# Performance work log

Measured on AMD Instinct MI355X. Metric: run time of the kernel, lower is better.

## Reference

```python
import jax, jax.numpy as jnp
import numpy as np

LOTRI2MAT = np.array([[0, 1, 3], [1, 2, 4], [3, 4, 5]])  # lower-tri 6-vec -> symmetric 3x3
MAT2LOTRI_I = np.array([0, 1, 1, 2, 2, 2])
MAT2LOTRI_J = np.array([0, 0, 1, 0, 1, 2])


def trilinear_warp_border(img, ddf):
    """MONAI Warp(mode='bilinear', padding_mode='border', align_corners=True).
    img: (B,C,H,W,D), ddf: (B,3,H,W,D) displacement in voxel units.
    Samples img at x + ddf(x), clamping coords to the volume (border padding).
    """
    B, C, H, W, D = img.shape
    base = jnp.stack(
        jnp.meshgrid(jnp.arange(H), jnp.arange(W), jnp.arange(D), indexing='ij'),
        axis=0,
    ).astype(img.dtype)  # (3,H,W,D)
    coords = ddf + base[None]  # (B,3,H,W,D)
    x = jnp.clip(coords[:, 0], 0.0, H - 1)
    y = jnp.clip(coords[:, 1], 0.0, W - 1)
    z = jnp.clip(coords[:, 2], 0.0, D - 1)

    x0f, y0f, z0f = jnp.floor(x), jnp.floor(y), jnp.floor(z)
    fx, fy, fz = x - x0f, y - y0f, z - z0f
    x0 = jnp.clip(x0f.astype(jnp.int32), 0, H - 1)
    y0 = jnp.clip(y0f.astype(jnp.int32), 0, W - 1)
    z0 = jnp.clip(z0f.astype(jnp.int32), 0, D - 1)
    x1 = jnp.minimum(x0 + 1, H - 1)
    y1 = jnp.minimum(y0 + 1, W - 1)
    z1 = jnp.minimum(z0 + 1, D - 1)

    def gather(img_b, xi, yi, zi):
        flat = (xi * W + yi) * D + zi  # (H,W,D)
        return img_b.reshape(C, -1)[:, flat.reshape(-1)].reshape(C, H, W, D)

    g = jax.vmap(gather)  # over batch

    out = jnp.zeros_like(img)
    for xi, wx in ((x0, 1.0 - fx), (x1, fx)):
        for yi, wy in ((y0, 1.0 - fy), (y1, fy)):
            for zi, wz in ((z0, 1.0 - fz), (z1, fz)):
                out = out + g(img, xi, yi, zi) * (wx * wy * wz)[:, None]
    return out


def jacobian_of_ddf(ddf):
    """J = I + du/dx via central differences (one-sided at boundaries).
    ddf: (B,3,H,W,D) -> (B,H,W,D,3,3) with J[...,i,j] = d u_i / d x_j + delta_ij."""
    grads = jnp.gradient(ddf, axis=(2, 3, 4))  # list over j of (B,3,H,W,D)
    J = jnp.stack(grads, axis=2)  # (B,3(i),3(j),H,W,D)
    J = J + jnp.eye(3, dtype=ddf.dtype)[None, :, :, None, None, None]
    return jnp.transpose(J, (0, 3, 4, 5, 1, 2))  # (B,H,W,D,3,3)


def setup_inputs() -> dict:
    key = jax.random.key(0)
    k1, k2 = jax.random.split(key)
    dti = jax.random.normal(k1, (2, 6, 64, 64, 64), dtype=jnp.float32)
    ddf = jax.random.normal(k2, (2, 3, 64, 64, 64), dtype=jnp.float32)
    return {"dti": dti, "ddf": ddf}


def reference(dti, ddf):
    b, _, h, w, d = dti.shape
    # 1) trilinear warp of the 6-channel lower-tri DTI
    dti_warped = trilinear_warp_border(dti, ddf)  # (B,6,H,W,D)
    # 2) lower-tri -> full symmetric 3x3, spatial-last
    M = dti_warped[:, LOTRI2MAT]                      # (B,3,3,H,W,D)
    M = jnp.transpose(M, (0, 3, 4, 5, 1, 2))          # (B,H,W,D,3,3)
    # 3) Jacobian of the deformation and its polar-decomposition rotation (finite strain)
    J = jacobian_of_ddf(ddf)                          # (B,H,W,D,3,3)
    U, _, Vh = jnp.linalg.svd(J, full_matrices=False)
    R = jnp.matmul(U, Vh)                             # orthogonal factor of J
    # 4) rotate tensors: R^T M R
    out = jnp.einsum('...ji,...jk,...kl->...il', R, M, R)
    # 5) back to lower-tri channel-first form
    out = jnp.transpose(out, (0, 4, 5, 1, 2, 3))      # (B,3,3,H,W,D)
    return out[:, MAT2LOTRI_I, MAT2LOTRI_J]           # (B,6,H,W,D)
```

## Files before the change

### kernel.cpp

```cpp
#include <hip/hip_runtime.h>

#define NVOX 262144
#define TOTAL (2 * NVOX)

typedef float f2u __attribute__((ext_vector_type(2), aligned(4)));

__global__ void zero_count(int* __restrict__ bad) {
    if (threadIdx.x == 0) bad[0] = 0;
}

__global__ __launch_bounds__(256)
void warp_main(const float* __restrict__ dti,
               const float* __restrict__ ddf,
               float* __restrict__ out,
               int* __restrict__ bad, int max_bad)
{
    const int idx = blockIdx.x * 256 + threadIdx.x;
    const int b = idx >> 18;
    const int r = idx & (NVOX - 1);
    const int x = r >> 12;
    const int y = (r >> 6) & 63;
    const int z = r & 63;

    const float* db = ddf + (size_t)b * 3 * NVOX;

    const float ux = db[r];
    const float uy = db[NVOX + r];
    const float uz = db[2 * NVOX + r];

    const float cx = fminf(fmaxf((float)x + ux, 0.0f), 63.0f);
    const float cy = fminf(fmaxf((float)y + uy, 0.0f), 63.0f);
    const float cz = fminf(fmaxf((float)z + uz, 0.0f), 63.0f);
    const float fx0 = floorf(cx), fy0 = floorf(cy), fz0 = floorf(cz);
    const float fx = cx - fx0, fy = cy - fy0, fz = cz - fz0;
    const int x0 = (int)fx0, y0 = (int)fy0, z0 = (int)fz0;
    const int x1 = min(x0 + 1, 63), y1 = min(y0 + 1, 63);

    const float gx = 1.0f - fx, gy = 1.0f - fy, gz = 1.0f - fz;
    const float q00 = gx * gy, q01 = gx * fy, q10 = fx * gy, q11 = fx * fy;

    const bool ztop = (z0 == 63);
    const int zb = ztop ? 62 : z0;
    const int p00 = (x0 * 64 + y0) * 64 + zb, p01 = (x0 * 64 + y1) * 64 + zb;
    const int p10 = (x1 * 64 + y0) * 64 + zb, p11 = (x1 * 64 + y1) * 64 + zb;

    const float* tb = dti + (size_t)b * 6 * NVOX;
    float m[6];
#pragma unroll
    for (int c = 0; c < 6; ++c) {
        const float* tc = tb + c * NVOX;
        const f2u v00 = *(const f2u*)(tc + p00);
        const f2u v01 = *(const f2u*)(tc + p01);
        const f2u v10 = *(const f2u*)(tc + p10);
        const f2u v11 = *(const f2u*)(tc + p11);
        const float l00 = (ztop ? v00.y : v00.x) * gz + v00.y * fz;
        const float l01 = (ztop ? v01.y : v01.x) * gz + v01.y * fz;
        const float l10 = (ztop ? v10.y : v10.x) * gz + v10.y * fz;
        const float l11 = (ztop ? v11.y : v11.x) * gz + v11.y * fz;
        m[c] = q00 * l00 + q01 * l01 + q10 * l10 + q11 * l11;
    }

    const int xm = max(x - 1, 0), xp = min(x + 1, 63);
    const int ym = max(y - 1, 0), yp = min(y + 1, 63);
    const int zm = max(z - 1, 0), zp = min(z + 1, 63);
    const float sx = (xp - xm == 2) ? 0.5f : 1.0f;
    const float sy = (yp - ym == 2) ? 0.5f : 1.0f;
    const float sz = (zp - zm == 2) ? 0.5f : 1.0f;

    float P[3][3];
#pragma unroll
    for (int i = 0; i < 3; ++i) {
        const float* ui = db + i * NVOX;
        const float ctr = (i == 0) ? ux : (i == 1) ? uy : uz;
        P[i][0] = (ui[(xp * 64 + y) * 64 + z] - ui[(xm * 64 + y) * 64 + z]) * sx
                + (i == 0 ? 1.0f : 0.0f);
        P[i][1] = (ui[(x * 64 + yp) * 64 + z] - ui[(x * 64 + ym) * 64 + z]) * sy
                + (i == 1 ? 1.0f : 0.0f);
        P[i][2] = (__shfl(ctr, zp) - __shfl(ctr, zm)) * sz + (i == 2 ? 1.0f : 0.0f);
    }

    float cond_est = 0.0f;
#pragma unroll
    for (int it = 0; it < 6; ++it) {
        const float C00 = P[1][1] * P[2][2] - P[1][2] * P[2][1];
        const float C01 = P[1][2] * P[2][0] - P[1][0] * P[2][2];
        const float C02 = P[1][0] * P[2][1] - P[1][1] * P[2][0];
        const float C10 = P[0][2] * P[2][1] - P[0][1] * P[2][2];
        const float C11 = P[0][0] * P[2][2] - P[0][2] * P[2][0];
        const float C12 = P[0][1] * P[2][0] - P[0][0] * P[2][1];
        const float C20 = P[0][1] * P[1][2] - P[0][2] * P[1][1];
        const float C21 = P[0][2] * P[1][0] - P[0][0] * P[1][2];
        const float C22 = P[0][0] * P[1][1] - P[0][1] * P[1][0];
        const float det = P[0][0] * C00 + P[0][1] * C01 + P[0][2] * C02;

        const float n2 = P[0][0]*P[0][0] + P[0][1]*P[0][1] + P[0][2]*P[0][2]
                       + P[1][0]*P[1][0] + P[1][1]*P[1][1] + P[1][2]*P[1][2]
                       + P[2][0]*P[2][0] + P[2][1]*P[2][1] + P[2][2]*P[2][2];
        const float a2 = C00*C00 + C01*C01 + C02*C02
                       + C10*C10 + C11*C11 + C12*C12
                       + C20*C20 + C21*C21 + C22*C22;

        const float ad = fmaxf(fabsf(det), 1e-30f);
        if (it == 0) cond_est = sqrtf(n2 * a2) / ad;

        const float t  = fmaxf(__builtin_amdgcn_sqrtf(a2 * __builtin_amdgcn_rcpf(n2)), 1e-20f);
        const float sg = (det < 0.0f) ? -1.0f : 1.0f;
        const float rt = __builtin_amdgcn_rsqf(t * ad);
        const float c1 = 0.5f * t * rt;
        const float c2 = 0.5f * sg * rt;

        P[0][0] = c1 * P[0][0] + c2 * C00;  P[0][1] = c1 * P[0][1] + c2 * C01;  P[0][2] = c1 * P[0][2] + c2 * C02;
        P[1][0] = c1 * P[1][0] + c2 * C10;  P[1][1] = c1 * P[1][1] + c2 * C11;  P[1][2] = c1 * P[1][2] + c2 * C12;
        P[2][0] = c1 * P[2][0] + c2 * C20;  P[2][1] = c1 * P[2][1] + c2 * C21;  P[2][2] = c1 * P[2][2] + c2 * C22;
    }

    const float M3[3][3] = {{m[0], m[1], m[3]},
                            {m[1], m[2], m[4]},
                            {m[3], m[4], m[5]}};
    float T[3][3];
#pragma unroll
    for (int i = 0; i < 3; ++i)
#pragma unroll
        for (int j = 0; j < 3; ++j)
            T[i][j] = P[0][i] * M3[0][j] + P[1][i] * M3[1][j] + P[2][i] * M3[2][j];

    float A[3][3];
#pragma unroll
    for (int i = 0; i < 3; ++i)
#pragma unroll
        for (int j = 0; j < 3; ++j)
            A[i][j] = T[i][0] * P[0][j] + T[i][1] * P[1][j] + T[i][2] * P[2][j];

    float* ob = out + (size_t)b * 6 * NVOX;
    ob[0 * NVOX + r] = A[0][0];
    ob[1 * NVOX + r] = A[1][0];
    ob[2 * NVOX + r] = A[1][1];
    ob[3 * NVOX + r] = A[2][0];
    ob[4 * NVOX + r] = A[2][1];
    ob[5 * NVOX + r] = A[2][2];

    if (cond_est > 1e4f) {
        const int slot = atomicAdd(bad, 1);
        if (slot < max_bad) bad[1 + slot] = idx;
    }
}

__global__ __launch_bounds__(256)
void rescue(const float* __restrict__ dti,
            const float* __restrict__ ddf,
            float* __restrict__ out,
            const int* __restrict__ bad, int max_bad)
{
    const int n = min(bad[0], max_bad);
    for (int k = blockIdx.x * 256 + threadIdx.x; k < n; k += 4 * 256) {
        const int idx = bad[1 + k];
        const int b = idx >> 18;
        const int r = idx & (NVOX - 1);
        const int x = r >> 12;
        const int y = (r >> 6) & 63;
        const int z = r & 63;

        const float* db = ddf + (size_t)b * 3 * NVOX;

        const float cx = fminf(fmaxf((float)x + db[r], 0.0f), 63.0f);
        const float cy = fminf(fmaxf((float)y + db[NVOX + r], 0.0f), 63.0f);
        const float cz = fminf(fmaxf((float)z + db[2 * NVOX + r], 0.0f), 63.0f);
        const float fx0 = floorf(cx), fy0 = floorf(cy), fz0 = floorf(cz);
        const float fx = cx - fx0, fy = cy - fy0, fz = cz - fz0;
        const int x0 = (int)fx0, y0 = (int)fy0, z0 = (int)fz0;
        const int x1 = min(x0 + 1, 63), y1 = min(y0 + 1, 63), z1 = min(z0 + 1, 63);
        const float gx = 1.0f - fx, gy = 1.0f - fy, gz = 1.0f - fz;
        const float w000 = gx*gy*gz, w001 = gx*gy*fz, w010 = gx*fy*gz, w011 = gx*fy*fz;
        const float w100 = fx*gy*gz, w101 = fx*gy*fz, w110 = fx*fy*gz, w111 = fx*fy*fz;
        const int o000 = (x0*64+y0)*64+z0, o001 = (x0*64+y0)*64+z1;
        const int o010 = (x0*64+y1)*64+z0, o011 = (x0*64+y1)*64+z1;
        const int o100 = (x1*64+y0)*64+z0, o101 = (x1*64+y0)*64+z1;
        const int o110 = (x1*64+y1)*64+z0, o111 = (x1*64+y1)*64+z1;

        const float* tb = dti + (size_t)b * 6 * NVOX;
        float m[6];
        for (int c = 0; c < 6; ++c) {
            const float* tc = tb + c * NVOX;
            m[c] = w000*tc[o000] + w001*tc[o001] + w010*tc[o010] + w011*tc[o011]
                 + w100*tc[o100] + w101*tc[o101] + w110*tc[o110] + w111*tc[o111];
        }

        const int xm = max(x-1,0), xp = min(x+1,63);
        const int ym = max(y-1,0), yp = min(y+1,63);
        const int zm = max(z-1,0), zp = min(z+1,63);
        const double sx = (xp-xm==2)?0.5:1.0, sy = (yp-ym==2)?0.5:1.0, sz = (zp-zm==2)?0.5:1.0;
        double X[3][3];
        for (int i = 0; i < 3; ++i) {
            const float* ui = db + i * NVOX;
            X[i][0] = ((double)ui[(xp*64+y)*64+z] - (double)ui[(xm*64+y)*64+z]) * sx + (i==0?1.0:0.0);
            X[i][1] = ((double)ui[(x*64+yp)*64+z] - (double)ui[(x*64+ym)*64+z]) * sy + (i==1?1.0:0.0);
            X[i][2] = ((double)ui[(x*64+y)*64+zp] - (double)ui[(x*64+y)*64+zm]) * sz + (i==2?1.0:0.0);
        }

        for (int it = 0; it < 14; ++it) {
            double mx = 0.0;
            for (int i = 0; i < 3; ++i)
                for (int j = 0; j < 3; ++j) mx = fmax(mx, fabs(X[i][j]));
            const double s = 1.0 / fmax(mx, 1e-300);
            for (int i = 0; i < 3; ++i)
                for (int j = 0; j < 3; ++j) X[i][j] *= s;

            const double C00 = X[1][1]*X[2][2] - X[1][2]*X[2][1];
            const double C01 = X[1][2]*X[2][0] - X[1][0]*X[2][2];
            const double C02 = X[1][0]*X[2][1] - X[1][1]*X[2][0];
            const double C10 = X[0][2]*X[2][1] - X[0][1]*X[2][2];
            const double C11 = X[0][0]*X[2][2] - X[0][2]*X[2][0];
            const double C12 = X[0][1]*X[2][0] - X[0][0]*X[2][1];
            const double C20 = X[0][1]*X[1][2] - X[0][2]*X[1][1];
            const double C21 = X[0][2]*X[1][0] - X[0][0]*X[1][2];
            const double C22 = X[0][0]*X[1][1] - X[0][1]*X[1][0];
            const double det = X[0][0]*C00 + X[0][1]*C01 + X[0][2]*C02;
            const double n2 = X[0][0]*X[0][0]+X[0][1]*X[0][1]+X[0][2]*X[0][2]
                            + X[1][0]*X[1][0]+X[1][1]*X[1][1]+X[1][2]*X[1][2]
                            + X[2][0]*X[2][0]+X[2][1]*X[2][1]+X[2][2]*X[2][2];
            const double a2 = C00*C00+C01*C01+C02*C02 + C10*C10+C11*C11+C12*C12
                            + C20*C20+C21*C21+C22*C22;
            const double t  = fmax(sqrt(a2 / n2), 1e-150);
            const double ad = fmax(fabs(det), 1e-280);
            const double sg = (det < 0.0) ? -1.0 : 1.0;
            const double c1 = 0.5 * sqrt(t / ad);
            const double c2 = 0.5 * sg / sqrt(t * ad);
            X[0][0]=c1*X[0][0]+c2*C00; X[0][1]=c1*X[0][1]+c2*C01; X[0][2]=c1*X[0][2]+c2*C02;
            X[1][0]=c1*X[1][0]+c2*C10; X[1][1]=c1*X[1][1]+c2*C11; X[1][2]=c1*X[1][2]+c2*C12;
            X[2][0]=c1*X[2][0]+c2*C20; X[2][1]=c1*X[2][1]+c2*C21; X[2][2]=c1*X[2][2]+c2*C22;
        }

        const double M3[3][3] = {{(double)m[0], (double)m[1], (double)m[3]},
                                 {(double)m[1], (double)m[2], (double)m[4]},
                                 {(double)m[3], (double)m[4], (double)m[5]}};
        double T[3][3], A[3][3];
        for (int i = 0; i < 3; ++i)
            for (int j = 0; j < 3; ++j)
                T[i][j] = X[0][i]*M3[0][j] + X[1][i]*M3[1][j] + X[2][i]*M3[2][j];
        for (int i = 0; i < 3; ++i)
            for (int j = 0; j < 3; ++j)
                A[i][j] = T[i][0]*X[0][j] + T[i][1]*X[1][j] + T[i][2]*X[2][j];

        float* ob = out + (size_t)b * 6 * NVOX;
        ob[0 * NVOX + r] = (float)A[0][0];
        ob[1 * NVOX + r] = (float)A[1][0];
        ob[2 * NVOX + r] = (float)A[1][1];
        ob[3 * NVOX + r] = (float)A[2][0];
        ob[4 * NVOX + r] = (float)A[2][1];
        ob[5 * NVOX + r] = (float)A[2][2];
    }
}

extern "C" void kernel_launch(void* const* d_in, const int* in_sizes, int n_in,
                              void* d_out, int out_size, void* d_ws, size_t ws_size,
                              hipStream_t stream) {
    const float* dti = (const float*)d_in[0];
    const float* ddf = (const float*)d_in[1];
    float* out = (float*)d_out;
    int* bad = (int*)d_ws;
    const int max_bad = (int)min((size_t)8192, ws_size / 4 - 1);

    zero_count<<<1, 64, 0, stream>>>(bad);
    warp_main<<<TOTAL / 256, 256, 0, stream>>>(dti, ddf, out, bad, max_bad);
    rescue<<<4, 256, 0, stream>>>(dti, ddf, out, bad, max_bad);
}
```

Baseline: 105.7 us.

## Replace atomic bad-voxel list with per-voxel flag array and full-grid rescue

Drops the zero-count kernel and the global atomic append list. Each voxel now writes a byte flag, and the condition check compares squared values so the sqrt and divide go away. A full-grid rescue kernel reads the flags, and a wave returns early when no lane is flagged. This removes one launch and the atomic contention, and it also lifts the 8192-entry cap. In exchange it adds a 512K-byte flag write and read plus a large launch that is mostly idle.

```diff
diff --git a/kernel.cpp b/kernel.cpp
--- a/kernel.cpp
+++ b/kernel.cpp
@@ -4,16 +4,12 @@
 #define TOTAL (2 * NVOX)
 
 typedef float f2u __attribute__((ext_vector_type(2), aligned(4)));
-
-__global__ void zero_count(int* __restrict__ bad) {
-    if (threadIdx.x == 0) bad[0] = 0;
-}
 
 __global__ __launch_bounds__(256)
 void warp_main(const float* __restrict__ dti,
                const float* __restrict__ ddf,
                float* __restrict__ out,
-               int* __restrict__ bad, int max_bad)
+               unsigned char* __restrict__ flags)
 {
     const int idx = blockIdx.x * 256 + threadIdx.x;
     const int b = idx >> 18;
@@ -79,7 +75,7 @@
         P[i][2] = (__shfl(ctr, zp) - __shfl(ctr, zm)) * sz + (i == 2 ? 1.0f : 0.0f);
     }
 
-    float cond_est = 0.0f;
+    bool need64 = false;
 #pragma unroll
     for (int it = 0; it < 6; ++it) {
         const float C00 = P[1][1] * P[2][2] - P[1][2] * P[2][1];
@@ -101,7 +97,7 @@
                        + C20*C20 + C21*C21 + C22*C22;
 
         const float ad = fmaxf(fabsf(det), 1e-30f);
-        if (it == 0) cond_est = sqrtf(n2 * a2) / ad;
+        if (it == 0) need64 = (n2 * a2 > 1e8f * ad * ad);
 
         const float t  = fmaxf(__builtin_amdgcn_sqrtf(a2 * __builtin_amdgcn_rcpf(n2)), 1e-20f);
         const float sg = (det < 0.0f) ? -1.0f : 1.0f;
@@ -139,116 +135,114 @@
     ob[4 * NVOX + r] = A[2][1];
     ob[5 * NVOX + r] = A[2][2];
 
-    if (cond_est > 1e4f) {
-        const int slot = atomicAdd(bad, 1);
-        if (slot < max_bad) bad[1 + slot] = idx;
-    }
+    flags[idx] = need64 ? 1 : 0;
 }
 
 __global__ __launch_bounds__(256)
-void rescue(const float* __restrict__ dti,
-            const float* __restrict__ ddf,
-            float* __restrict__ out,
-            const int* __restrict__ bad, int max_bad)
+void rescue_flag(const float* __restrict__ dti,
+                 const float* __restrict__ ddf,
+                 float* __restrict__ out,
+                 const unsigned char* __restrict__ flags)
 {
-    const int n = min(bad[0], max_bad);
-    for (int k = blockIdx.x * 256 + threadIdx.x; k < n; k += 4 * 256) {
-        const int idx = bad[1 + k];
-        const int b = idx >> 18;
-        const int r = idx & (NVOX - 1);
-        const int x = r >> 12;
-        const int y = (r >> 6) & 63;
-        const int z = r & 63;
-
-        const float* db = ddf + (size_t)b * 3 * NVOX;
-
-        const float cx = fminf(fmaxf((float)x + db[r], 0.0f), 63.0f);
-        const float cy = fminf(fmaxf((float)y + db[NVOX + r], 0.0f), 63.0f);
-        const float cz = fminf(fmaxf((float)z + db[2 * NVOX + r], 0.0f), 63.0f);
-        const float fx0 = floorf(cx), fy0 = floorf(cy), fz0 = floorf(cz);
-        const float fx = cx - fx0, fy = cy - fy0, fz = cz - fz0;
-        const int x0 = (int)fx0, y0 = (int)fy0, z0 = (int)fz0;
-        const int x1 = min(x0 + 1, 63), y1 = min(y0 + 1, 63), z1 = min(z0 + 1, 63);
-        const float gx = 1.0f - fx, gy = 1.0f - fy, gz = 1.0f - fz;
-        const float w000 = gx*gy*gz, w001 = gx*gy*fz, w010 = gx*fy*gz, w011 = gx*fy*fz;
-        const float w100 = fx*gy*gz, w101 = fx*gy*fz, w110 = fx*fy*gz, w111 = fx*fy*fz;
-        const int o000 = (x0*64+y0)*64+z0, o001 = (x0*64+y0)*64+z1;
-        const int o010 = (x0*64+y1)*64+z0, o011 = (x0*64+y1)*64+z1;
-        const int o100 = (x1*64+y0)*64+z0, o101 = (x1*64+y0)*64+z1;
-        const int o110 = (x1*64+y1)*64+z0, o111 = (x1*64+y1)*64+z1;
-
-        const float* tb = dti + (size_t)b * 6 * NVOX;
-        float m[6];
-        for (int c = 0; c < 6; ++c) {
-            const float* tc = tb + c * NVOX;
-            m[c] = w000*tc[o000] + w001*tc[o001] + w010*tc[o010] + w011*tc[o011]
-                 + w100*tc[o100] + w101*tc[o101] + w110*tc[o110] + w111*tc[o111];
-        }
-
-        const int xm = max(x-1,0), xp = min(x+1,63);
-        const int ym = max(y-1,0), yp = min(y+1,63);
-        const int zm = max(z-1,0), zp = min(z+1,63);
-        const double sx = (xp-xm==2)?0.5:1.0, sy = (yp-ym==2)?0.5:1.0, sz = (zp-zm==2)?0.5:1.0;
-        double X[3][3];
-        for (int i = 0; i < 3; ++i) {
-            const float* ui = db + i * NVOX;
-            X[i][0] = ((double)ui[(xp*64+y)*64+z] - (double)ui[(xm*64+y)*64+z]) * sx + (i==0?1.0:0.0);
-            X[i][1] = ((double)ui[(x*64+yp)*64+z] - (double)ui[(x*64+ym)*64+z]) * sy + (i==1?1.0:0.0);
-            X[i][2] = ((double)ui[(x*64+y)*64+zp] - (double)ui[(x*64+y)*64+zm]) * sz + (i==2?1.0:0.0);
-        }
-
-        for (int it = 0; it < 14; ++it) {
-            double mx = 0.0;
-            for (int i = 0; i < 3; ++i)
-                for (int j = 0; j < 3; ++j) mx = fmax(mx, fabs(X[i][j]));
-            const double s = 1.0 / fmax(mx, 1e-300);
-            for (int i = 0; i < 3; ++i)
-                for (int j = 0; j < 3; ++j) X[i][j] *= s;
-
-            const double C00 = X[1][1]*X[2][2] - X[1][2]*X[2][1];
-            const double C01 = X[1][2]*X[2][0] - X[1][0]*X[2][2];
-            const double C02 = X[1][0]*X[2][1] - X[1][1]*X[2][0];
-            const double C10 = X[0][2]*X[2][1] - X[0][1]*X[2][2];
-            const double C11 = X[0][0]*X[2][2] - X[0][2]*X[2][0];
-            const double C12 = X[0][1]*X[2][0] - X[0][0]*X[2][1];
-            const double C20 = X[0][1]*X[1][2] - X[0][2]*X[1][1];
-            const double C21 = X[0][2]*X[1][0] - X[0][0]*X[1][2];
-            const double C22 = X[0][0]*X[1][1] - X[0][1]*X[1][0];
-            const double det = X[0][0]*C00 + X[0][1]*C01 + X[0][2]*C02;
-            const double n2 = X[0][0]*X[0][0]+X[0][1]*X[0][1]+X[0][2]*X[0][2]
-                            + X[1][0]*X[1][0]+X[1][1]*X[1][1]+X[1][2]*X[1][2]
-                            + X[2][0]*X[2][0]+X[2][1]*X[2][1]+X[2][2]*X[2][2];
-            const double a2 = C00*C00+C01*C01+C02*C02 + C10*C10+C11*C11+C12*C12
-                            + C20*C20+C21*C21+C22*C22;
-            const double t  = fmax(sqrt(a2 / n2), 1e-150);
-            const double ad = fmax(fabs(det), 1e-280);
-            const double sg = (det < 0.0) ? -1.0 : 1.0;
-            const double c1 = 0.5 * sqrt(t / ad);
-            const double c2 = 0.5 * sg / sqrt(t * ad);
-            X[0][0]=c1*X[0][0]+c2*C00; X[0][1]=c1*X[0][1]+c2*C01; X[0][2]=c1*X[0][2]+c2*C02;
-            X[1][0]=c1*X[1][0]+c2*C10; X[1][1]=c1*X[1][1]+c2*C11; X[1][2]=c1*X[1][2]+c2*C12;
-            X[2][0]=c1*X[2][0]+c2*C20; X[2][1]=c1*X[2][1]+c2*C21; X[2][2]=c1*X[2][2]+c2*C22;
-        }
-
-        const double M3[3][3] = {{(double)m[0], (double)m[1], (double)m[3]},
-                                 {(double)m[1], (double)m[2], (double)m[4]},
-                                 {(double)m[3], (double)m[4], (double)m[5]}};
-        double T[3][3], A[3][3];
+    const int idx = blockIdx.x * 256 + threadIdx.x;
+    const bool mine = (flags[idx] != 0);
+    if (__ballot(mine) == 0ull) return;
+    if (!mine) return;
+
+    const int b = idx >> 18;
+    const int r = idx & (NVOX - 1);
+    const int x = r >> 12;
+    const int y = (r >> 6) & 63;
+    const int z = r & 63;
+
+    const float* db = ddf + (size_t)b * 3 * NVOX;
+
+    const float cx = fminf(fmaxf((float)x + db[r], 0.0f), 63.0f);
+    const float cy = fminf(fmaxf((float)y + db[NVOX + r], 0.0f), 63.0f);
+    const float cz = fminf(fmaxf((float)z + db[2 * NVOX + r], 0.0f), 63.0f);
+    const float fx0 = floorf(cx), fy0 = floorf(cy), fz0 = floorf(cz);
+    const float fx = cx - fx0, fy = cy - fy0, fz = cz - fz0;
+    const int x0 = (int)fx0, y0 = (int)fy0, z0 = (int)fz0;
+    const int x1 = min(x0 + 1, 63), y1 = min(y0 + 1, 63), z1 = min(z0 + 1, 63);
+    const float gx = 1.0f - fx, gy = 1.0f - fy, gz = 1.0f - fz;
+    const float w000 = gx*gy*gz, w001 = gx*gy*fz, w010 = gx*fy*gz, w011 = gx*fy*fz;
+    const float w100 = fx*gy*gz, w101 = fx*gy*fz, w110 = fx*fy*gz, w111 = fx*fy*fz;
+    const int o000 = (x0*64+y0)*64+z0, o001 = (x0*64+y0)*64+z1;
+    const int o010 = (x0*64+y1)*64+z0, o011 = (x0*64+y1)*64+z1;
+    const int o100 = (x1*64+y0)*64+z0, o101 = (x1*64+y0)*64+z1;
+    const int o110 = (x1*64+y1)*64+z0, o111 = (x1*64+y1)*64+z1;
+
+    const float* tb = dti + (size_t)b * 6 * NVOX;
+    float m[6];
+    for (int c = 0; c < 6; ++c) {
+        const float* tc = tb + c * NVOX;
+        m[c] = w000*tc[o000] + w001*tc[o001] + w010*tc[o010] + w011*tc[o011]
+             + w100*tc[o100] + w101*tc[o101] + w110*tc[o110] + w111*tc[o111];
+    }
+
+    const int xm = max(x-1,0), xp = min(x+1,63);
+    const int ym = max(y-1,0), yp = min(y+1,63);
+    const int zm = max(z-1,0), zp = min(z+1,63);
+    const double sx = (xp-xm==2)?0.5:1.0, sy = (yp-ym==2)?0.5:1.0, sz = (zp-zm==2)?0.5:1.0;
+    double X[3][3];
+    for (int i = 0; i < 3; ++i) {
+        const float* ui = db + i * NVOX;
+        X[i][0] = ((double)ui[(xp*64+y)*64+z] - (double)ui[(xm*64+y)*64+z]) * sx + (i==0?1.0:0.0);
+        X[i][1] = ((double)ui[(x*64+yp)*64+z] - (double)ui[(x*64+ym)*64+z]) * sy + (i==1?1.0:0.0);
+        X[i][2] = ((double)ui[(x*64+y)*64+zp] - (double)ui[(x*64+y)*64+zm]) * sz + (i==2?1.0:0.0);
+    }
+
+    for (int it = 0; it < 14; ++it) {
+        double mx = 0.0;
         for (int i = 0; i < 3; ++i)
-            for (int j = 0; j < 3; ++j)
-                T[i][j] = X[0][i]*M3[0][j] + X[1][i]*M3[1][j] + X[2][i]*M3[2][j];
+            for (int j = 0; j < 3; ++j) mx = fmax(mx, fabs(X[i][j]));
+        const double s = 1.0 / fmax(mx, 1e-300);
         for (int i = 0; i < 3; ++i)
-            for (int j = 0; j < 3; ++j)
-                A[i][j] = T[i][0]*X[0][j] + T[i][1]*X[1][j] + T[i][2]*X[2][j];
-
-        float* ob = out + (size_t)b * 6 * NVOX;
-        ob[0 * NVOX + r] = (float)A[0][0];
-        ob[1 * NVOX + r] = (float)A[1][0];
-        ob[2 * NVOX + r] = (float)A[1][1];
-        ob[3 * NVOX + r] = (float)A[2][0];
-        ob[4 * NVOX + r] = (float)A[2][1];
-        ob[5 * NVOX + r] = (float)A[2][2];
-    }
+            for (int j = 0; j < 3; ++j) X[i][j] *= s;
+
+        const double C00 = X[1][1]*X[2][2] - X[1][2]*X[2][1];
+        const double C01 = X[1][2]*X[2][0] - X[1][0]*X[2][2];
+        const double C02 = X[1][0]*X[2][1] - X[1][1]*X[2][0];
+        const double C10 = X[0][2]*X[2][1] - X[0][1]*X[2][2];
+        const double C11 = X[0][0]*X[2][2] - X[0][2]*X[2][0];
+        const double C12 = X[0][1]*X[2][0] - X[0][0]*X[2][1];
+        const double C20 = X[0][1]*X[1][2] - X[0][2]*X[1][1];
+        const double C21 = X[0][2]*X[1][0] - X[0][0]*X[1][2];
+        const double C22 = X[0][0]*X[1][1] - X[0][1]*X[1][0];
+        const double det = X[0][0]*C00 + X[0][1]*C01 + X[0][2]*C02;
+        const double n2 = X[0][0]*X[0][0]+X[0][1]*X[0][1]+X[0][2]*X[0][2]
+                        + X[1][0]*X[1][0]+X[1][1]*X[1][1]+X[1][2]*X[1][2]
+                        + X[2][0]*X[2][0]+X[2][1]*X[2][1]+X[2][2]*X[2][2];
+        const double a2 = C00*C00+C01*C01+C02*C02 + C10*C10+C11*C11+C12*C12
+                        + C20*C20+C21*C21+C22*C22;
+        const double t  = fmax(sqrt(a2 / n2), 1e-150);
+        const double ad = fmax(fabs(det), 1e-280);
+        const double sg = (det < 0.0) ? -1.0 : 1.0;
+        const double c1 = 0.5 * sqrt(t / ad);
+        const double c2 = 0.5 * sg / sqrt(t * ad);
+        X[0][0]=c1*X[0][0]+c2*C00; X[0][1]=c1*X[0][1]+c2*C01; X[0][2]=c1*X[0][2]+c2*C02;
+        X[1][0]=c1*X[1][0]+c2*C10; X[1][1]=c1*X[1][1]+c2*C11; X[1][2]=c1*X[1][2]+c2*C12;
+        X[2][0]=c1*X[2][0]+c2*C20; X[2][1]=c1*X[2][1]+c2*C21; X[2][2]=c1*X[2][2]+c2*C22;
+    }
+
+    const double M3[3][3] = {{(double)m[0], (double)m[1], (double)m[3]},
+                             {(double)m[1], (double)m[2], (double)m[4]},
+                             {(double)m[3], (double)m[4], (double)m[5]}};
+    double T[3][3], A[3][3];
+    for (int i = 0; i < 3; ++i)
+        for (int j = 0; j < 3; ++j)
+            T[i][j] = X[0][i]*M3[0][j] + X[1][i]*M3[1][j] + X[2][i]*M3[2][j];
+    for (int i = 0; i < 3; ++i)
+        for (int j = 0; j < 3; ++j)
+            A[i][j] = T[i][0]*X[0][j] + T[i][1]*X[1][j] + T[i][2]*X[2][j];
+
+    float* ob = out + (size_t)b * 6 * NVOX;
+    ob[0 * NVOX + r] = (float)A[0][0];
+    ob[1 * NVOX + r] = (float)A[1][0];
+    ob[2 * NVOX + r] = (float)A[1][1];
+    ob[3 * NVOX + r] = (float)A[2][0];
+    ob[4 * NVOX + r] = (float)A[2][1];
+    ob[5 * NVOX + r] = (float)A[2][2];
 }
 
 extern "C" void kernel_launch(void* const* d_in, const int* in_sizes, int n_in,
@@ -257,10 +251,8 @@
     const float* dti = (const float*)d_in[0];
     const float* ddf = (const float*)d_in[1];
     float* out = (float*)d_out;
-    int* bad = (int*)d_ws;
-    const int max_bad = (int)min((size_t)8192, ws_size / 4 - 1);
-
-    zero_count<<<1, 64, 0, stream>>>(bad);
-    warp_main<<<TOTAL / 256, 256, 0, stream>>>(dti, ddf, out, bad, max_bad);
-    rescue<<<4, 256, 0, stream>>>(dti, ddf, out, bad, max_bad);
+    unsigned char* flags = (unsigned char*)d_ws;
+
+    warp_main<<<TOTAL / 256, 256, 0, stream>>>(dti, ddf, out, flags);
+    rescue_flag<<<TOTAL / 256, 256, 0, stream>>>(dti, ddf, out, flags);
 }
```

After: 107.3 us. No clear change (+1.5%).
